# Optimization experiments

Measured on AMD Instinct MI355X. Metric: run time of the kernel, lower is better.

Reference implementation:

```python
import jax, jax.numpy as jnp
import numpy as np

N_HEADS = 16
HEAD = 64
SEQ = 2048
EMBED = 1024
BATCH = 4

def setup_inputs() -> dict:
    key = jax.random.key(0)
    ks = jax.random.split(key, 6)
    inputs = jax.random.normal(ks[0], (BATCH, SEQ, EMBED), dtype=jnp.float32)
    # per-head projection weights stacked: [H, E, D] (nn.Linear(E, D, bias=False))
    s = 1.0 / np.sqrt(EMBED)
    Wq = jax.random.uniform(ks[1], (N_HEADS, EMBED, HEAD), jnp.float32, -s, s)
    Wk = jax.random.uniform(ks[2], (N_HEADS, EMBED, HEAD), jnp.float32, -s, s)
    Wv = jax.random.uniform(ks[3], (N_HEADS, EMBED, HEAD), jnp.float32, -s, s)
    Wo = jax.random.uniform(ks[4], (EMBED, EMBED), jnp.float32, -s, s)
    bo = jax.random.uniform(ks[5], (EMBED,), jnp.float32, -s, s)
    return {"inputs": inputs, "Wq": Wq, "Wk": Wk, "Wv": Wv, "Wo": Wo, "bo": bo}

def reference(inputs, Wq, Wk, Wv, Wo, bo):
    B, S, E = inputs.shape
    # batched per-head projections: [B,S,E] x [H,E,D] -> [B,H,S,D]
    q = jnp.einsum('bse,hed->bhsd', inputs, Wq)
    k = jnp.einsum('bse,hed->bhsd', inputs, Wk)
    v = jnp.einsum('bse,hed->bhsd', inputs, Wv)
    q = q / jnp.sqrt(jnp.float32(HEAD)).astype(q.dtype)
    scores = jnp.einsum('bhsd,bhtd->bhst', q, k)  # [B,H,S,S]
    causal = jnp.tril(jnp.ones((S, S), dtype=bool))
    scores = jnp.where(causal, scores, jnp.finfo(scores.dtype).min)
    weights = jax.nn.softmax(scores, axis=-1)
    out = jnp.einsum('bhst,bhtd->bhsd', weights, v)  # [B,H,S,D]
    # concat heads in head order -> [B,S,H*D]
    out = jnp.transpose(out, (0, 2, 1, 3)).reshape(B, S, N_HEADS * HEAD)
    return out @ Wo.T + bo
```

## Files before the change

kernel.cpp:

```cpp
#include <hip/hip_runtime.h>
#include <stdint.h>

typedef unsigned short ushort_t;
typedef __attribute__((ext_vector_type(8))) short short8;
typedef __attribute__((ext_vector_type(4))) short bf16x4;
typedef __attribute__((ext_vector_type(4))) float f32x4;

#define AS1 __attribute__((address_space(1)))
#define AS3 __attribute__((address_space(3)))

__device__ __forceinline__ void gl_lds16(const void* g, void* l) {
    __builtin_amdgcn_global_load_lds((const AS1 unsigned int*)g,
                                     (AS3 unsigned int*)l, 16, 0, 0);
}

__device__ __forceinline__ ushort_t f2bf(float f) {
    union { float f; unsigned u; } v; v.f = f;
    unsigned r = v.u + 0x7fffu + ((v.u >> 16) & 1u);
    return (ushort_t)(r >> 16);
}

__device__ __forceinline__ unsigned cvt_pk_bf16(float lo, float hi) {
    unsigned r;
    asm("v_cvt_pk_bf16_f32 %0, %1, %2" : "=v"(r) : "v"(lo), "v"(hi));
    return r;
}

__global__ __launch_bounds__(256) void prep_k(const float* __restrict__ inp,
                                              const float* __restrict__ Wo,
                                              const float* __restrict__ Wq,
                                              const float* __restrict__ Wk,
                                              const float* __restrict__ Wv,
                                              ushort_t* __restrict__ inp_bf,
                                              ushort_t* __restrict__ WoB,
                                              ushort_t* __restrict__ WT) {
    const int bx = blockIdx.x, tid = threadIdx.x;
    if (bx < 4608) {
        const float* src = (bx < 4096) ? inp : Wo;
        ushort_t* dst    = (bx < 4096) ? inp_bf : WoB;
        int i = ((bx < 4096 ? bx : bx - 4096) * 256 + tid) * 8;
        float4 a = *(const float4*)(src + i);
        float4 b = *(const float4*)(src + i + 4);
        short8 o;
        o[0] = (short)f2bf(a.x); o[1] = (short)f2bf(a.y);
        o[2] = (short)f2bf(a.z); o[3] = (short)f2bf(a.w);
        o[4] = (short)f2bf(b.x); o[5] = (short)f2bf(b.y);
        o[6] = (short)f2bf(b.z); o[7] = (short)f2bf(b.w);
        *(short8*)(dst + i) = o;
        return;
    }
    __shared__ ushort_t t[64 * 65];
    const int wb = bx - 4608;
    const int mat = wb >> 8;
    const int h   = (wb >> 4) & 15;
    const int et  = wb & 15;
    const float* W = (mat == 0 ? Wq : (mat == 1 ? Wk : Wv)) + h * (1024 * 64);
    const float* src = W + et * 64 * 64;
#pragma unroll
    for (int i = 0; i < 16; ++i) {
        int idx = i * 256 + tid;
        int e = idx >> 6, d = idx & 63;
        t[e * 65 + d] = f2bf(src[idx]);
    }
    __syncthreads();
    ushort_t* dst = WT + (mat * 16 + h) * (64 * 1024) + et * 64;
#pragma unroll
    for (int i = 0; i < 16; ++i) {
        int idx = i * 256 + tid;
        int d = idx >> 6, e = idx & 63;
        dst[d * 1024 + e] = t[e * 65 + d];
    }
}

__global__ __launch_bounds__(512, 4) void qkv_k(const ushort_t* __restrict__ A,
                                                const ushort_t* __restrict__ WT,
                                                ushort_t* __restrict__ Q,
                                                ushort_t* __restrict__ K,
                                                ushort_t* __restrict__ Vt) {
    __shared__ __align__(16) ushort_t ring[36864];
    const int tid = threadIdx.x, wave = tid >> 6, lane = tid & 63;
    const int ln15 = lane & 15, quad = lane >> 4;
    const int wm = wave >> 1, wn = wave & 1;
    const int m0 = blockIdx.x * 256, n0 = blockIdx.y * 128;

    const int sa_row  = wave * 16 + (lane >> 2);
    const int sa_colS = (((lane & 3) ^ ((lane >> 3) & 3))) * 8;
    const int woff    = wave * 512;
    const int rchunk  = (quad ^ ((ln15 >> 1) & 3)) * 8;

    f32x4 acc[4][4];
#pragma unroll
    for (int i = 0; i < 4; ++i)
#pragma unroll
        for (int j = 0; j < 4; ++j)
#pragma unroll
            for (int e = 0; e < 4; ++e) acc[i][j][e] = 0.f;

    auto stage = [&](int t, ushort_t* buf) {
        const int kb = t * 32;
        gl_lds16(A  + (size_t)(m0 + sa_row)       * 1024 + kb + sa_colS, buf + woff);
        gl_lds16(A  + (size_t)(m0 + 128 + sa_row) * 1024 + kb + sa_colS, buf + 4096 + woff);
        gl_lds16(WT + (size_t)(n0 + sa_row)       * 1024 + kb + sa_colS, buf + 8192 + woff);
    };

    stage(0, &ring[0]); stage(1, &ring[12288]);
    asm volatile("s_waitcnt vmcnt(3)" ::: "memory");
    __builtin_amdgcn_s_barrier();
    __builtin_amdgcn_sched_barrier(0);

    auto phase = [&](int t, const ushort_t* bufC, ushort_t* bufS) {
        short8 a[4], b[4];
#pragma unroll
        for (int f = 0; f < 4; ++f)
            a[f] = *(const short8*)&bufC[(wm * 64 + f * 16 + ln15) * 32 + rchunk];
#pragma unroll
        for (int f = 0; f < 4; ++f)
            b[f] = *(const short8*)&bufC[8192 + (wn * 64 + f * 16 + ln15) * 32 + rchunk];
        if (t + 2 < 32) stage(t + 2, bufS);
        if (t < 30)       asm volatile("s_waitcnt vmcnt(3)" ::: "memory");
        else if (t == 30) asm volatile("s_waitcnt vmcnt(0)" ::: "memory");
        __builtin_amdgcn_sched_barrier(0);
        __builtin_amdgcn_s_setprio(1);
#pragma unroll
        for (int fm = 0; fm < 4; ++fm)
#pragma unroll
            for (int fn = 0; fn < 4; ++fn)
                acc[fm][fn] = __builtin_amdgcn_mfma_f32_16x16x32_bf16(a[fm], b[fn], acc[fm][fn], 0, 0, 0);
        __builtin_amdgcn_s_setprio(0);
        __builtin_amdgcn_s_barrier();
        __builtin_amdgcn_sched_barrier(0);
    };

    for (int t3 = 0; t3 < 30; t3 += 3) {
        phase(t3,     &ring[0],     &ring[24576]);
        phase(t3 + 1, &ring[12288], &ring[0]);
        phase(t3 + 2, &ring[24576], &ring[12288]);
    }
    phase(30, &ring[0],     &ring[24576]);
    phase(31, &ring[12288], &ring[0]);

    const int n_base = n0 + wn * 64;
    const int mat = n_base >> 10;
    const int h   = (n_base >> 6) & 15;
    if (mat < 2) {
        ushort_t* dst = (mat == 0) ? Q : K;
        const float scale = (mat == 0) ? 0.125f : 1.0f;
#pragma unroll
        for (int fm = 0; fm < 4; ++fm) {
#pragma unroll
            for (int r = 0; r < 4; ++r) {
                int mg = m0 + wm * 64 + fm * 16 + quad * 4 + r;
                int bi = mg >> 11, s = mg & 2047;
                size_t base = ((size_t)(bi * 16 + h) * 2048 + s) * 64;
#pragma unroll
                for (int fn = 0; fn < 4; ++fn)
                    dst[base + fn * 16 + ln15] = f2bf(acc[fm][fn][r] * scale);
            }
        }
    } else {
        ushort_t* tb = &ring[wave * 4608];
#pragma unroll
        for (int fn = 0; fn < 4; ++fn)
#pragma unroll
            for (int fm = 0; fm < 4; ++fm) {
                uint2 w;
                w.x = cvt_pk_bf16(acc[fm][fn][0], acc[fm][fn][1]);
                w.y = cvt_pk_bf16(acc[fm][fn][2], acc[fm][fn][3]);
                *(uint2*)&tb[(fn * 16 + ln15) * 72 + fm * 16 + quad * 4] = w;
            }
        const int s0 = m0 + wm * 64;
        const int bi = s0 >> 11, sb = s0 & 2047;
#pragma unroll
        for (int p = 0; p < 8; ++p) {
            int d  = p * 8 + (lane >> 3);
            int sc = (lane & 7) * 8;
            short8 vv = *(const short8*)&tb[d * 72 + sc];
            *(short8*)&Vt[((size_t)(bi * 16 + h) * 64 + d) * 2048 + sb + sc] = vv;
        }
    }
}

__global__ __launch_bounds__(256, 3) void flash_k(const ushort_t* Q, const ushort_t* K,
                                                  const ushort_t* Vt, ushort_t* Aout) {
    __shared__ __align__(16) ushort_t Ks[2][64 * 64];
    __shared__ __align__(16) ushort_t Vts[2][64 * 64];
    __shared__ __align__(16) ushort_t PT[4][32 * 72];
    const int tid = threadIdx.x, wave = tid >> 6, lane = tid & 63;
    const int ln15 = lane & 15, quad = lane >> 4;
    const int bx = blockIdx.x;
    const int qt = 15 - (bx >> 6);
    const int bh = bx & 63;
    const int qw = qt * 128 + wave * 32;
    const ushort_t* Kb = K + (size_t)bh * 2048 * 64;
    const ushort_t* Vb = Vt + (size_t)bh * 64 * 2048;
    ushort_t* myPT = PT[wave];
    const int srow = tid >> 3, c8 = (tid & 7) * 8;
    const int c8s  = ((tid & 7) ^ ((tid >> 3) & 7)) * 8;
    const int swr  = ln15 & 7;

    short8 qf[2][2];
    {
        const ushort_t* Qb = Q + (size_t)bh * 2048 * 64;
#pragma unroll
        for (int qs = 0; qs < 2; ++qs)
#pragma unroll
            for (int kk = 0; kk < 2; ++kk)
                qf[qs][kk] = *(const short8*)&Qb[(size_t)(qw + qs * 16 + ln15) * 64 + kk * 32 + quad * 8];
    }

    f32x4 o[4][2];
#pragma unroll
    for (int dt = 0; dt < 4; ++dt)
#pragma unroll
        for (int qs = 0; qs < 2; ++qs)
#pragma unroll
            for (int e = 0; e < 4; ++e) o[dt][qs][e] = 0.f;
    float l_s[2] = {0.f, 0.f};

    const int ktEnd = 2 * qt + 2;
    gl_lds16(Kb + (size_t)srow * 64 + c8s,        &Ks[0][srow * 64 + c8]);
    gl_lds16(Kb + (size_t)(32 + srow) * 64 + c8s, &Ks[0][(32 + srow) * 64 + c8]);
    gl_lds16(Vb + (size_t)srow * 2048 + c8s,        &Vts[0][srow * 64 + c8]);
    gl_lds16(Vb + (size_t)(32 + srow) * 2048 + c8s, &Vts[0][(32 + srow) * 64 + c8]);
    __syncthreads();

    for (int kt = 0; kt < ktEnd; ++kt) {
        const int cur = kt & 1, nxt = cur ^ 1;
        if (kt + 1 < ktEnd) {
            int kn = kt + 1;
            gl_lds16(Kb + (size_t)(kn * 64 + srow) * 64 + c8s,      &Ks[nxt][srow * 64 + c8]);
            gl_lds16(Kb + (size_t)(kn * 64 + 32 + srow) * 64 + c8s, &Ks[nxt][(32 + srow) * 64 + c8]);
            gl_lds16(Vb + (size_t)srow * 2048 + kn * 64 + c8s,        &Vts[nxt][srow * 64 + c8]);
            gl_lds16(Vb + (size_t)(32 + srow) * 2048 + kn * 64 + c8s, &Vts[nxt][(32 + srow) * 64 + c8]);
        }
        if (kt * 64 <= qw + 31) {
            f32x4 sc[4][2];
#pragma unroll
            for (int ks = 0; ks < 4; ++ks) {
#pragma unroll
                for (int qs = 0; qs < 2; ++qs)
#pragma unroll
                    for (int e = 0; e < 4; ++e) sc[ks][qs][e] = 0.f;
            }
            __builtin_amdgcn_s_setprio(1);
#pragma unroll
            for (int ks = 0; ks < 4; ++ks) {
#pragma unroll
                for (int kk = 0; kk < 2; ++kk) {
                    short8 kf = *(const short8*)&Ks[cur][(ks * 16 + ln15) * 64 + ((kk * 4 + quad) ^ swr) * 8];
#pragma unroll
                    for (int qs = 0; qs < 2; ++qs)
                        sc[ks][qs] = __builtin_amdgcn_mfma_f32_16x16x32_bf16(kf, qf[qs][kk], sc[ks][qs], 0, 0, 0);
                }
            }
            __builtin_amdgcn_s_setprio(0);
            if (kt * 64 + 63 > qw) {
#pragma unroll
                for (int ks = 0; ks < 4; ++ks)
#pragma unroll
                    for (int qs = 0; qs < 2; ++qs) {
                        int qg = qw + qs * 16 + ln15;
#pragma unroll
                        for (int r = 0; r < 4; ++r) {
                            int kg = kt * 64 + ks * 16 + quad * 4 + r;
                            if (kg > qg) sc[ks][qs][r] = -1e30f;
                        }
                    }
            }
#pragma unroll
            for (int qs = 0; qs < 2; ++qs) {
#pragma unroll
                for (int ks = 0; ks < 4; ++ks) {
                    float p0 = __expf(sc[ks][qs][0]);
                    float p1 = __expf(sc[ks][qs][1]);
                    float p2 = __expf(sc[ks][qs][2]);
                    float p3 = __expf(sc[ks][qs][3]);
                    l_s[qs] += (p0 + p1) + (p2 + p3);
                    uint2 w;
                    w.x = cvt_pk_bf16(p0, p1);
                    w.y = cvt_pk_bf16(p2, p3);
                    *(uint2*)&myPT[(qs * 16 + ln15) * 72 + ks * 16 + quad * 4] = w;
                }
            }
            short8 pf[2][2];
#pragma unroll
            for (int qs = 0; qs < 2; ++qs)
#pragma unroll
                for (int kk = 0; kk < 2; ++kk)
                    pf[qs][kk] = *(const short8*)&myPT[(qs * 16 + ln15) * 72 + kk * 32 + quad * 8];
            __builtin_amdgcn_s_setprio(1);
#pragma unroll
            for (int dt = 0; dt < 4; ++dt)
#pragma unroll
                for (int kk = 0; kk < 2; ++kk) {
                    short8 vf = *(const short8*)&Vts[cur][(dt * 16 + ln15) * 64 + ((kk * 4 + quad) ^ swr) * 8];
#pragma unroll
                    for (int qs = 0; qs < 2; ++qs)
                        o[dt][qs] = __builtin_amdgcn_mfma_f32_16x16x32_bf16(vf, pf[qs][kk], o[dt][qs], 0, 0, 0);
                }
            __builtin_amdgcn_s_setprio(0);
        }
        __syncthreads();
    }
#pragma unroll
    for (int qs = 0; qs < 2; ++qs) {
        float l = l_s[qs];
        l += __shfl_xor(l, 16);
        l += __shfl_xor(l, 32);
        float inv = 1.f / l;
#pragma unroll
        for (int dt = 0; dt < 4; ++dt) {
            uint2 w;
            w.x = cvt_pk_bf16(o[dt][qs][0] * inv, o[dt][qs][1] * inv);
            w.y = cvt_pk_bf16(o[dt][qs][2] * inv, o[dt][qs][3] * inv);
            *(uint2*)&myPT[(qs * 16 + ln15) * 72 + dt * 16 + quad * 4] = w;
        }
    }
    const int bi = bh >> 4, h = bh & 15;
#pragma unroll
    for (int p = 0; p < 4; ++p) {
        int row = p * 8 + (lane >> 3);
        int cc = (lane & 7) * 8;
        short8 vv = *(const short8*)&myPT[row * 72 + cc];
        int qg = qw + row;
        *(short8*)&Aout[((size_t)bi * 2048 + qg) * 1024 + h * 64 + cc] = vv;
    }
}

__global__ __launch_bounds__(512, 4) void outproj_k(const ushort_t* __restrict__ A,
                                                    const ushort_t* __restrict__ WoB,
                                                    const float* __restrict__ bo,
                                                    float* __restrict__ Out) {
    __shared__ __align__(16) ushort_t ring[36864];
    const int tid = threadIdx.x, wave = tid >> 6, lane = tid & 63;
    const int ln15 = lane & 15, quad = lane >> 4;
    const int wm = wave >> 1, wn = wave & 1;
    const int m0 = blockIdx.x * 256, n0 = blockIdx.y * 128;

    const int sa_row  = wave * 16 + (lane >> 2);
    const int sa_colS = (((lane & 3) ^ ((lane >> 3) & 3))) * 8;
    const int woff    = wave * 512;
    const int rchunk  = (quad ^ ((ln15 >> 1) & 3)) * 8;

    f32x4 acc[4][4];
#pragma unroll
    for (int i = 0; i < 4; ++i)
#pragma unroll
        for (int j = 0; j < 4; ++j)
#pragma unroll
            for (int e = 0; e < 4; ++e) acc[i][j][e] = 0.f;

    auto stage = [&](int t, ushort_t* buf) {
        const int kb = t * 32;
        gl_lds16(A   + (size_t)(m0 + sa_row)       * 1024 + kb + sa_colS, buf + woff);
        gl_lds16(A   + (size_t)(m0 + 128 + sa_row) * 1024 + kb + sa_colS, buf + 4096 + woff);
        gl_lds16(WoB + (size_t)(n0 + sa_row)       * 1024 + kb + sa_colS, buf + 8192 + woff);
    };

    stage(0, &ring[0]); stage(1, &ring[12288]);
    asm volatile("s_waitcnt vmcnt(3)" ::: "memory");
    __builtin_amdgcn_s_barrier();
    __builtin_amdgcn_sched_barrier(0);

    auto phase = [&](int t, const ushort_t* bufC, ushort_t* bufS) {
        short8 a[4], b[4];
#pragma unroll
        for (int f = 0; f < 4; ++f)
            a[f] = *(const short8*)&bufC[(wm * 64 + f * 16 + ln15) * 32 + rchunk];
#pragma unroll
        for (int f = 0; f < 4; ++f)
            b[f] = *(const short8*)&bufC[8192 + (wn * 64 + f * 16 + ln15) * 32 + rchunk];
        if (t + 2 < 32) stage(t + 2, bufS);
        if (t < 30)       asm volatile("s_waitcnt vmcnt(3)" ::: "memory");
        else if (t == 30) asm volatile("s_waitcnt vmcnt(0)" ::: "memory");
        __builtin_amdgcn_sched_barrier(0);
        __builtin_amdgcn_s_setprio(1);
#pragma unroll
        for (int fm = 0; fm < 4; ++fm)
#pragma unroll
            for (int fn = 0; fn < 4; ++fn)
                acc[fm][fn] = __builtin_amdgcn_mfma_f32_16x16x32_bf16(a[fm], b[fn], acc[fm][fn], 0, 0, 0);
        __builtin_amdgcn_s_setprio(0);
        __builtin_amdgcn_s_barrier();
        __builtin_amdgcn_sched_barrier(0);
    };

    for (int t3 = 0; t3 < 30; t3 += 3) {
        phase(t3,     &ring[0],     &ring[24576]);
        phase(t3 + 1, &ring[12288], &ring[0]);
        phase(t3 + 2, &ring[24576], &ring[12288]);
    }
    phase(30, &ring[0],     &ring[24576]);
    phase(31, &ring[12288], &ring[0]);

    const int nb = n0 + wn * 64;
    float bias[4];
#pragma unroll
    for (int fn = 0; fn < 4; ++fn) bias[fn] = bo[nb + fn * 16 + ln15];
#pragma unroll
    for (int fm = 0; fm < 4; ++fm)
#pragma unroll
        for (int r = 0; r < 4; ++r) {
            int mg = m0 + wm * 64 + fm * 16 + quad * 4 + r;
#pragma unroll
            for (int fn = 0; fn < 4; ++fn)
                Out[(size_t)mg * 1024 + nb + fn * 16 + ln15] = acc[fm][fn][r] + bias[fn];
        }
}

extern "C" void kernel_launch(void* const* d_in, const int* in_sizes, int n_in,
                              void* d_out, int out_size, void* d_ws, size_t ws_size,
                              hipStream_t stream) {
    (void)in_sizes; (void)n_in; (void)out_size; (void)ws_size;
    const float* inp = (const float*)d_in[0];
    const float* Wq  = (const float*)d_in[1];
    const float* Wk  = (const float*)d_in[2];
    const float* Wv  = (const float*)d_in[3];
    const float* Wo  = (const float*)d_in[4];
    const float* bo  = (const float*)d_in[5];
    float* out = (float*)d_out;

    ushort_t* ws = (ushort_t*)d_ws;
    ushort_t* R0  = ws;
    ushort_t* WT  = R0  + 8388608;
    ushort_t* WoB = WT  + 3145728;
    ushort_t* Qb  = WoB + 1048576;
    ushort_t* Kb  = Qb  + 8388608;
    ushort_t* Vtb = Kb  + 8388608;

    ushort_t* inp_bf = R0;
    ushort_t* At     = R0;

    prep_k<<<5376, 256, 0, stream>>>(inp, Wo, Wq, Wk, Wv, inp_bf, WoB, WT);
    qkv_k<<<dim3(32, 24), 512, 0, stream>>>(inp_bf, WT, Qb, Kb, Vtb);
    flash_k<<<dim3(1024), 256, 0, stream>>>(Qb, Kb, Vtb, At);
    outproj_k<<<dim3(32, 8), 512, 0, stream>>>(At, WoB, bo, out);
}
```

Measured before the change: 216.5 us.

## Switch flash attention to 32x32 MFMA with register-resident P via permlane swap

The attention inner loop now uses 32x32x16 bf16 MFMA tiles, with each wave owning 32 query rows as a single tile instead of 16x16 sub-tiles. The probability matrix is repacked into the B-operand layout using v_permlane32_swap within registers rather than being written to and reread from a per-wave LDS buffer. Removing that LDS buffer lets the output staging reuse the K/V buffer and allows a launch bound of 4 blocks per CU instead of 3. The aim is fewer LDS round trips and fewer MFMA issues per tile. The risks are higher register pressure from 16-wide accumulators under the tighter occupancy target, and the correctness of the lane mapping after the swap.

Result: no change. 216.2 us, median of 2 (-0.1%).

```diff
diff --git a/kernel.cpp b/kernel.cpp
--- a/kernel.cpp
+++ b/kernel.cpp
@@ -5,6 +5,7 @@
 typedef __attribute__((ext_vector_type(8))) short short8;
 typedef __attribute__((ext_vector_type(4))) short bf16x4;
 typedef __attribute__((ext_vector_type(4))) float f32x4;
+typedef __attribute__((ext_vector_type(16))) float f32x16;
 
 #define AS1 __attribute__((address_space(1)))
 #define AS3 __attribute__((address_space(3)))
@@ -180,150 +181,134 @@
     }
 }
 
-__global__ __launch_bounds__(256, 3) void flash_k(const ushort_t* Q, const ushort_t* K,
+__global__ __launch_bounds__(256, 4) void flash_k(const ushort_t* Q, const ushort_t* K,
                                                   const ushort_t* Vt, ushort_t* Aout) {
-    __shared__ __align__(16) ushort_t Ks[2][64 * 64];
-    __shared__ __align__(16) ushort_t Vts[2][64 * 64];
-    __shared__ __align__(16) ushort_t PT[4][32 * 72];
+    __shared__ __align__(16) ushort_t KVs[2][2][64 * 64];
     const int tid = threadIdx.x, wave = tid >> 6, lane = tid & 63;
-    const int ln15 = lane & 15, quad = lane >> 4;
+    const int ln31 = lane & 31, h = lane >> 5;
     const int bx = blockIdx.x;
     const int qt = 15 - (bx >> 6);
     const int bh = bx & 63;
     const int qw = qt * 128 + wave * 32;
     const ushort_t* Kb = K + (size_t)bh * 2048 * 64;
     const ushort_t* Vb = Vt + (size_t)bh * 64 * 2048;
-    ushort_t* myPT = PT[wave];
     const int srow = tid >> 3, c8 = (tid & 7) * 8;
     const int c8s  = ((tid & 7) ^ ((tid >> 3) & 7)) * 8;
-    const int swr  = ln15 & 7;
-
-    short8 qf[2][2];
+    const int swr  = ln31 & 7;
+
+    short8 qf[4];
     {
         const ushort_t* Qb = Q + (size_t)bh * 2048 * 64;
 #pragma unroll
-        for (int qs = 0; qs < 2; ++qs)
-#pragma unroll
-            for (int kk = 0; kk < 2; ++kk)
-                qf[qs][kk] = *(const short8*)&Qb[(size_t)(qw + qs * 16 + ln15) * 64 + kk * 32 + quad * 8];
-    }
-
-    f32x4 o[4][2];
-#pragma unroll
-    for (int dt = 0; dt < 4; ++dt)
-#pragma unroll
-        for (int qs = 0; qs < 2; ++qs)
-#pragma unroll
-            for (int e = 0; e < 4; ++e) o[dt][qs][e] = 0.f;
-    float l_s[2] = {0.f, 0.f};
+        for (int c = 0; c < 4; ++c)
+            qf[c] = *(const short8*)&Qb[(size_t)(qw + ln31) * 64 + c * 16 + h * 8];
+    }
+
+    f32x16 o[2];
+#pragma unroll
+    for (int dt = 0; dt < 2; ++dt)
+#pragma unroll
+        for (int e = 0; e < 16; ++e) o[dt][e] = 0.f;
+    float l_s = 0.f;
 
     const int ktEnd = 2 * qt + 2;
-    gl_lds16(Kb + (size_t)srow * 64 + c8s,        &Ks[0][srow * 64 + c8]);
-    gl_lds16(Kb + (size_t)(32 + srow) * 64 + c8s, &Ks[0][(32 + srow) * 64 + c8]);
-    gl_lds16(Vb + (size_t)srow * 2048 + c8s,        &Vts[0][srow * 64 + c8]);
-    gl_lds16(Vb + (size_t)(32 + srow) * 2048 + c8s, &Vts[0][(32 + srow) * 64 + c8]);
+    gl_lds16(Kb + (size_t)srow * 64 + c8s,          &KVs[0][0][srow * 64 + c8]);
+    gl_lds16(Kb + (size_t)(32 + srow) * 64 + c8s,   &KVs[0][0][(32 + srow) * 64 + c8]);
+    gl_lds16(Vb + (size_t)srow * 2048 + c8s,        &KVs[0][1][srow * 64 + c8]);
+    gl_lds16(Vb + (size_t)(32 + srow) * 2048 + c8s, &KVs[0][1][(32 + srow) * 64 + c8]);
     __syncthreads();
 
     for (int kt = 0; kt < ktEnd; ++kt) {
         const int cur = kt & 1, nxt = cur ^ 1;
         if (kt + 1 < ktEnd) {
             int kn = kt + 1;
-            gl_lds16(Kb + (size_t)(kn * 64 + srow) * 64 + c8s,      &Ks[nxt][srow * 64 + c8]);
-            gl_lds16(Kb + (size_t)(kn * 64 + 32 + srow) * 64 + c8s, &Ks[nxt][(32 + srow) * 64 + c8]);
-            gl_lds16(Vb + (size_t)srow * 2048 + kn * 64 + c8s,        &Vts[nxt][srow * 64 + c8]);
-            gl_lds16(Vb + (size_t)(32 + srow) * 2048 + kn * 64 + c8s, &Vts[nxt][(32 + srow) * 64 + c8]);
+            gl_lds16(Kb + (size_t)(kn * 64 + srow) * 64 + c8s,        &KVs[nxt][0][srow * 64 + c8]);
+            gl_lds16(Kb + (size_t)(kn * 64 + 32 + srow) * 64 + c8s,   &KVs[nxt][0][(32 + srow) * 64 + c8]);
+            gl_lds16(Vb + (size_t)srow * 2048 + kn * 64 + c8s,        &KVs[nxt][1][srow * 64 + c8]);
+            gl_lds16(Vb + (size_t)(32 + srow) * 2048 + kn * 64 + c8s, &KVs[nxt][1][(32 + srow) * 64 + c8]);
         }
         if (kt * 64 <= qw + 31) {
-            f32x4 sc[4][2];
-#pragma unroll
-            for (int ks = 0; ks < 4; ++ks) {
-#pragma unroll
-                for (int qs = 0; qs < 2; ++qs)
-#pragma unroll
-                    for (int e = 0; e < 4; ++e) sc[ks][qs][e] = 0.f;
-            }
-            __builtin_amdgcn_s_setprio(1);
-#pragma unroll
-            for (int ks = 0; ks < 4; ++ks) {
-#pragma unroll
-                for (int kk = 0; kk < 2; ++kk) {
-                    short8 kf = *(const short8*)&Ks[cur][(ks * 16 + ln15) * 64 + ((kk * 4 + quad) ^ swr) * 8];
-#pragma unroll
-                    for (int qs = 0; qs < 2; ++qs)
-                        sc[ks][qs] = __builtin_amdgcn_mfma_f32_16x16x32_bf16(kf, qf[qs][kk], sc[ks][qs], 0, 0, 0);
+            const ushort_t* Ksc = KVs[cur][0];
+            const ushort_t* Vsc = KVs[cur][1];
+            unsigned W[2][8];
+            const bool diag = (kt * 64 + 63 > qw);
+            const int qg = qw + ln31;
+#pragma unroll
+            for (int kt2 = 0; kt2 < 2; ++kt2) {
+                f32x16 sc;
+#pragma unroll
+                for (int e = 0; e < 16; ++e) sc[e] = 0.f;
+                __builtin_amdgcn_s_setprio(1);
+#pragma unroll
+                for (int c = 0; c < 4; ++c) {
+                    short8 kf = *(const short8*)&Ksc[(kt2 * 32 + ln31) * 64 + ((2 * c + h) ^ swr) * 8];
+                    sc = __builtin_amdgcn_mfma_f32_32x32x16_bf16(kf, qf[c], sc, 0, 0, 0);
+                }
+                __builtin_amdgcn_s_setprio(0);
+                if (diag) {
+#pragma unroll
+                    for (int r = 0; r < 16; ++r) {
+                        int kg = kt * 64 + kt2 * 32 + (r & 3) + 8 * (r >> 2) + 4 * h;
+                        if (kg > qg) sc[r] = -1e30f;
+                    }
+                }
+#pragma unroll
+                for (int g = 0; g < 4; ++g) {
+                    float p0 = __expf(sc[4 * g + 0]);
+                    float p1 = __expf(sc[4 * g + 1]);
+                    float p2 = __expf(sc[4 * g + 2]);
+                    float p3 = __expf(sc[4 * g + 3]);
+                    l_s += (p0 + p1) + (p2 + p3);
+                    W[kt2][2 * g]     = cvt_pk_bf16(p0, p1);
+                    W[kt2][2 * g + 1] = cvt_pk_bf16(p2, p3);
                 }
             }
-            __builtin_amdgcn_s_setprio(0);
-            if (kt * 64 + 63 > qw) {
-#pragma unroll
-                for (int ks = 0; ks < 4; ++ks)
-#pragma unroll
-                    for (int qs = 0; qs < 2; ++qs) {
-                        int qg = qw + qs * 16 + ln15;
-#pragma unroll
-                        for (int r = 0; r < 4; ++r) {
-                            int kg = kt * 64 + ks * 16 + quad * 4 + r;
-                            if (kg > qg) sc[ks][qs][r] = -1e30f;
-                        }
-                    }
-            }
-#pragma unroll
-            for (int qs = 0; qs < 2; ++qs) {
-#pragma unroll
-                for (int ks = 0; ks < 4; ++ks) {
-                    float p0 = __expf(sc[ks][qs][0]);
-                    float p1 = __expf(sc[ks][qs][1]);
-                    float p2 = __expf(sc[ks][qs][2]);
-                    float p3 = __expf(sc[ks][qs][3]);
-                    l_s[qs] += (p0 + p1) + (p2 + p3);
-                    uint2 w;
-                    w.x = cvt_pk_bf16(p0, p1);
-                    w.y = cvt_pk_bf16(p2, p3);
-                    *(uint2*)&myPT[(qs * 16 + ln15) * 72 + ks * 16 + quad * 4] = w;
+            short8 pb[4];
+#pragma unroll
+            for (int t = 0; t < 2; ++t)
+#pragma unroll
+                for (int x = 0; x < 2; ++x) {
+                    unsigned a0 = W[t][4 * x + 0], b0 = W[t][4 * x + 2];
+                    unsigned a1 = W[t][4 * x + 1], b1 = W[t][4 * x + 3];
+                    asm volatile("v_permlane32_swap_b32 %0, %1" : "+v"(a0), "+v"(b0));
+                    asm volatile("v_permlane32_swap_b32 %0, %1" : "+v"(a1), "+v"(b1));
+                    union { unsigned u[4]; short8 s; } u;
+                    u.u[0] = a0; u.u[1] = a1; u.u[2] = b0; u.u[3] = b1;
+                    pb[t * 2 + x] = u.s;
                 }
-            }
-            short8 pf[2][2];
-#pragma unroll
-            for (int qs = 0; qs < 2; ++qs)
-#pragma unroll
-                for (int kk = 0; kk < 2; ++kk)
-                    pf[qs][kk] = *(const short8*)&myPT[(qs * 16 + ln15) * 72 + kk * 32 + quad * 8];
             __builtin_amdgcn_s_setprio(1);
 #pragma unroll
-            for (int dt = 0; dt < 4; ++dt)
-#pragma unroll
-                for (int kk = 0; kk < 2; ++kk) {
-                    short8 vf = *(const short8*)&Vts[cur][(dt * 16 + ln15) * 64 + ((kk * 4 + quad) ^ swr) * 8];
-#pragma unroll
-                    for (int qs = 0; qs < 2; ++qs)
-                        o[dt][qs] = __builtin_amdgcn_mfma_f32_16x16x32_bf16(vf, pf[qs][kk], o[dt][qs], 0, 0, 0);
+            for (int dt = 0; dt < 2; ++dt)
+#pragma unroll
+                for (int x = 0; x < 4; ++x) {
+                    short8 vf = *(const short8*)&Vsc[(dt * 32 + ln31) * 64 + ((2 * x + h) ^ swr) * 8];
+                    o[dt] = __builtin_amdgcn_mfma_f32_32x32x16_bf16(vf, pb[x], o[dt], 0, 0, 0);
                 }
             __builtin_amdgcn_s_setprio(0);
         }
         __syncthreads();
     }
-#pragma unroll
-    for (int qs = 0; qs < 2; ++qs) {
-        float l = l_s[qs];
-        l += __shfl_xor(l, 16);
-        l += __shfl_xor(l, 32);
-        float inv = 1.f / l;
-#pragma unroll
-        for (int dt = 0; dt < 4; ++dt) {
-            uint2 w;
-            w.x = cvt_pk_bf16(o[dt][qs][0] * inv, o[dt][qs][1] * inv);
-            w.y = cvt_pk_bf16(o[dt][qs][2] * inv, o[dt][qs][3] * inv);
-            *(uint2*)&myPT[(qs * 16 + ln15) * 72 + dt * 16 + quad * 4] = w;
-        }
-    }
-    const int bi = bh >> 4, h = bh & 15;
+    l_s += __shfl_xor(l_s, 32);
+    float inv = 1.f / l_s;
+    ushort_t* myO = &KVs[0][0][0] + wave * 2304;
+#pragma unroll
+    for (int dt = 0; dt < 2; ++dt)
+#pragma unroll
+        for (int g = 0; g < 4; ++g) {
+            unsigned w0 = cvt_pk_bf16(o[dt][4 * g + 0] * inv, o[dt][4 * g + 1] * inv);
+            unsigned w1 = cvt_pk_bf16(o[dt][4 * g + 2] * inv, o[dt][4 * g + 3] * inv);
+            int d0 = 8 * g + 4 * h + 32 * dt;
+            *(unsigned*)&myO[ln31 * 72 + d0]     = w0;
+            *(unsigned*)&myO[ln31 * 72 + d0 + 2] = w1;
+        }
+    const int bi = bh >> 4, hh = bh & 15;
 #pragma unroll
     for (int p = 0; p < 4; ++p) {
         int row = p * 8 + (lane >> 3);
         int cc = (lane & 7) * 8;
-        short8 vv = *(const short8*)&myPT[row * 72 + cc];
-        int qg = qw + row;
-        *(short8*)&Aout[((size_t)bi * 2048 + qg) * 1024 + h * 64 + cc] = vv;
+        short8 vv = *(const short8*)&myO[row * 72 + cc];
+        int qg2 = qw + row;
+        *(short8*)&Aout[((size_t)bi * 2048 + qg2) * 1024 + hh * 64 + cc] = vv;
     }
 }
 
```
